# Kernel tuning notes

Hardware: AMD Instinct MI355X
Metric: run time of the kernel (lower is better)

Reference implementation:

```python
import jax, jax.numpy as jnp
import numpy as np

B, SEQ_LEN, CHANNELS, PRED_LEN = 64, 1024, 512, 720
KERNEL = 25
PAD = (KERNEL - 1) // 2  # 12
IN_LEN = SEQ_LEN // 2    # 512
INV_SQRT2 = 1.0 / np.sqrt(2.0).astype(np.float32)


def dct2_ortho_matrix(N):
    # Orthonormal DCT-II basis: X_k = s_k * sum_n x_n cos(pi*(n+0.5)*k/N)
    n = np.arange(N, dtype=np.float64)
    k = np.arange(N, dtype=np.float64)
    M = np.cos(np.pi * (n[None, :] + 0.5) * k[:, None] / N)
    scale = np.sqrt(2.0 / N) * np.ones(N)
    scale[0] = np.sqrt(1.0 / N)
    return jnp.asarray((scale[:, None] * M).astype(np.float32))  # [k, n]


def setup_inputs() -> dict:
    key = jax.random.key(0)
    k1, k2, k3, k4, k5 = jax.random.split(key, 5)
    bound = 1.0 / np.sqrt(IN_LEN)
    return {
        "x": jax.random.normal(k1, (B, SEQ_LEN, CHANNELS), dtype=jnp.float32),
        "W_seasonal": jax.random.uniform(k2, (PRED_LEN, IN_LEN), jnp.float32, -bound, bound),
        "b_seasonal": jax.random.uniform(k3, (PRED_LEN,), jnp.float32, -bound, bound),
        "W_trend": jax.random.uniform(k4, (PRED_LEN, IN_LEN), jnp.float32, -bound, bound),
        "b_trend": jax.random.uniform(k5, (PRED_LEN,), jnp.float32, -bound, bound),
    }


def reference(x, W_seasonal, b_seasonal, W_trend, b_trend):
    # --- series decomposition: moving average (edge-padded, window 25) ---
    padded = jnp.pad(x, ((0, 0), (PAD, PAD), (0, 0)), mode="edge")  # [B, L+24, C]
    cs = jnp.cumsum(padded, axis=1)
    cs = jnp.pad(cs, ((0, 0), (1, 0), (0, 0)))  # leading zero, [B, L+25, C]
    trend = (cs[:, KERNEL:, :] - cs[:, :-KERNEL, :]) / KERNEL  # [B, L, C]
    seasonal = x - trend

    # [B, C, L]
    s = jnp.transpose(seasonal, (0, 2, 1))
    t = jnp.transpose(trend, (0, 2, 1))

    # --- grouped conv1d with [1,1]/sqrt(2), stride 2 (Haar low-pass downsample) ---
    def down(v):
        return (v[..., 0::2] + v[..., 1::2]) * INV_SQRT2  # [B, C, L/2]

    s = down(s)
    t = down(t)

    # --- orthonormal DCT-II over last axis, then divide by length ---
    Mdct = dct2_ortho_matrix(IN_LEN)  # [k, n]
    s = jnp.einsum("bcn,kn->bck", s, Mdct) / IN_LEN
    t = jnp.einsum("bcn,kn->bck", t, Mdct) / IN_LEN

    # --- shared Linear per branch ---
    s_out = jnp.einsum("bck,pk->bcp", s, W_seasonal) + b_seasonal
    t_out = jnp.einsum("bck,pk->bcp", t, W_trend) + b_trend

    out = s_out + t_out  # [B, C, pred_len]
    return jnp.transpose(out, (0, 2, 1))  # [B, pred_len, C]
```

## Files before the change

kernel.cpp:

```cpp
#include <hip/hip_runtime.h>
#include <hip/hip_bf16.h>
#include <math.h>


#define BATCH 64
#define SEQ 1024
#define CH 512
#define PRED 720
#define INV_SQRT2 0.70710678118654752440f

typedef __attribute__((ext_vector_type(4))) float floatx4;
typedef __attribute__((ext_vector_type(8))) short bf16x8;

#define KBF_OFF   0ull
#define BIAS_OFF  1572864ull
#define MW_OFF    1575936ull
#define WEFFS_OFF 2624512ull
#define WEFFT_OFF 4099072ull
#define XT_OFF    5573632ull
#define WS_NEED   (XT_OFF + 67108864ull)

__global__ void build_M(float* __restrict__ Mw) {
    int idx = blockIdx.x * 256 + threadIdx.x;
    int k = idx >> 9, n = idx & 511;
    int m = ((2 * n + 1) * k) & 2047;
    float ang = (float)m * (float)(M_PI / 1024.0);
    float scale = (k == 0) ? 0.04419417382415922f
                           : 0.0625f;
    Mw[idx] = cosf(ang) * scale * (1.0f / 512.0f);
}

__global__ void __launch_bounds__(256) build_weff(
    const float* __restrict__ Ws_in, const float* __restrict__ Wt_in,
    const float* __restrict__ Mw,
    float* __restrict__ outS, float* __restrict__ outT) {
    const float* W = blockIdx.z ? Wt_in : Ws_in;
    float* out     = blockIdx.z ? outT  : outS;
    int n0 = blockIdx.x * 64;
    int p0 = blockIdx.y * 64;
    int t  = threadIdx.x;
    int tx = t & 15, ty = t >> 4;
    __shared__ float wlds[32][65];
    __shared__ float mlds[32][64];
    float a[4][4] = {};
    for (int kb = 0; kb < 512; kb += 32) {
        __syncthreads();
        {
            int pp = t >> 2, kk0 = (t & 3) * 8;
            int prow = min(p0 + pp, PRED - 1);
            const float* wsrc = &W[(size_t)prow * 512 + kb + kk0];
#pragma unroll
            for (int e = 0; e < 8; e++) wlds[kk0 + e][pp] = wsrc[e];
        }
        {
            int kk = t >> 3, nn = (t & 7) * 8;
            const float* msrc = &Mw[(size_t)(kb + kk) * 512 + n0 + nn];
            *reinterpret_cast<floatx4*>(&mlds[kk][nn])     = *reinterpret_cast<const floatx4*>(&msrc[0]);
            *reinterpret_cast<floatx4*>(&mlds[kk][nn + 4]) = *reinterpret_cast<const floatx4*>(&msrc[4]);
        }
        __syncthreads();
#pragma unroll
        for (int kk = 0; kk < 32; kk++) {
            floatx4 wv = *reinterpret_cast<const floatx4*>(&wlds[kk][ty * 4]);
            floatx4 mv = *reinterpret_cast<const floatx4*>(&mlds[kk][tx * 4]);
#pragma unroll
            for (int i = 0; i < 4; i++)
#pragma unroll
                for (int j = 0; j < 4; j++)
                    a[i][j] += wv[i] * mv[j];
        }
    }
#pragma unroll
    for (int i = 0; i < 4; i++) {
        int p = p0 + ty * 4 + i;
        if (p < PRED) {
            floatx4 v = {a[i][0], a[i][1], a[i][2], a[i][3]};
            *reinterpret_cast<floatx4*>(&out[(size_t)p * 512 + n0 + tx * 4]) = v;
        }
    }
}

__device__ __forceinline__ int tcnt(int j, int l) {
    if (l == 0)    return max(0, 13 - j);
    if (l == 1023) return max(0, j - 1010);
    int d = l - j; if (d < 0) d = -d;
    return (d <= 12) ? 1 : 0;
}

__global__ void build_kmat(const float* __restrict__ Ws, const float* __restrict__ Wt,
                           const float* __restrict__ bs, const float* __restrict__ bt,
                           __hip_bfloat16* __restrict__ Kbf, float* __restrict__ bias) {
    int idx = blockIdx.x * 256 + threadIdx.x;
    int p = idx >> 10, l = idx & 1023;
    if (p >= PRED) { Kbf[idx] = __float2bfloat16(0.0f); return; }
    if (l == 0) bias[p] = bs[p] + bt[p];
    float v = INV_SQRT2 * Ws[(size_t)p * 512 + (l >> 1)];
    int jlo = max(0, l - 12), jhi = min(1023, l + 12);
    float acc = 0.f;
    for (int n = (jlo >> 1); n <= (jhi >> 1); n++) {
        int c = tcnt(2 * n, l) + tcnt(2 * n + 1, l);
        if (c) acc += (Wt[(size_t)p * 512 + n] - Ws[(size_t)p * 512 + n]) * (float)c;
    }
    v += acc * (INV_SQRT2 / 25.0f);
    Kbf[idx] = __float2bfloat16(v);
}

__device__ __forceinline__ void async_ld16(const void* g, void* l) {
    __builtin_amdgcn_global_load_lds((const __attribute__((address_space(1))) void*)g,
                                     (__attribute__((address_space(3))) void*)l, 16, 0, 0);
}

__device__ __forceinline__ short f2bf(float f) {
    __hip_bfloat16 h = __float2bfloat16(f);
    return *reinterpret_cast<short*>(&h);
}

__global__ void __launch_bounds__(256) xpose(const float* __restrict__ x,
                                             short* __restrict__ xT) {
    __shared__ float lds[64][65];
    int t = threadIdx.x;
    int l0 = blockIdx.x * 64, c0 = blockIdx.y * 64, b = blockIdx.z;
    const float* xb = x + (size_t)b * SEQ * CH;
    int row4 = t >> 4, cq = t & 15;
#pragma unroll
    for (int i = 0; i < 4; i++) {
        int row = row4 + i * 16;
        floatx4 v = *reinterpret_cast<const floatx4*>(
            xb + (size_t)(l0 + row) * CH + c0 + cq * 4);
#pragma unroll
        for (int e = 0; e < 4; e++) lds[row][cq * 4 + e] = v[e];
    }
    __syncthreads();
    size_t outb = (size_t)b * CH * SEQ;
#pragma unroll
    for (int r = 0; r < 2; r++) {
        int u = r * 256 + t;
        int lr = u & 7, c = u >> 3;
        bf16x8 s;
#pragma unroll
        for (int e = 0; e < 8; e++) s[e] = f2bf(lds[lr * 8 + e][c]);
        *reinterpret_cast<bf16x8*>(&xT[outb + (size_t)(c0 + c) * SEQ + l0 + lr * 8]) = s;
    }
}

__global__ void __launch_bounds__(256, 4) gemm_main_t(
    const short* __restrict__ Kbf, const short* __restrict__ xT,
    const float* __restrict__ bias, float* __restrict__ out) {
    __shared__ __align__(16) short ldsbuf[2 * 2 * 128 * 32];
    int t = threadIdx.x;
    int wave = t >> 6, lane = t & 63;
    int bid = blockIdx.x;
    int work = (bid & 7) * 192 + (bid >> 3);
    int mt = work % 6;
    int grp = work / 6;
    int nt = grp & 3, b = grp >> 2;
    int wm = wave >> 1, wn = wave & 1;
    const short* Ag = Kbf + (size_t)mt * 128 * 1024;
    const short* Bg = xT + ((size_t)b * CH + nt * 128) * 1024;

    size_t srcoff[2];
#pragma unroll
    for (int rdi = 0; rdi < 2; rdi++) {
        int q = rdi * 256 + t;
        int row = ((q >> 6) << 4) + (q & 15);
        int ko = ((q >> 4) & 3) * 8;
        srcoff[rdi] = (size_t)row * 1024 + ko;
    }

    floatx4 acc[4][4];
#pragma unroll
    for (int i = 0; i < 4; i++)
#pragma unroll
        for (int j = 0; j < 4; j++)
            acc[i][j] = (floatx4){0.f, 0.f, 0.f, 0.f};

#pragma unroll
    for (int rdi = 0; rdi < 2; rdi++) {
        char* dA = (char*)ldsbuf + rdi * 4096 + wave * 1024;
        async_ld16(Ag + srcoff[rdi], dA);
        async_ld16(Bg + srcoff[rdi], dA + 8192);
    }
    __syncthreads();

    int cur = 0;
    for (int it = 0; it < 32; ++it) {
        if (it < 31) {
            int k0n = (it + 1) * 32;
            char* base = (char*)ldsbuf + (cur ^ 1) * 16384;
#pragma unroll
            for (int rdi = 0; rdi < 2; rdi++) {
                char* dA = base + rdi * 4096 + wave * 1024;
                async_ld16(Ag + srcoff[rdi] + k0n, dA);
                async_ld16(Bg + srcoff[rdi] + k0n, dA + 8192);
            }
        }
        const char* cb = (const char*)ldsbuf + cur * 16384;
        bf16x8 af[4], bf[4];
#pragma unroll
        for (int i = 0; i < 4; i++)
            af[i] = *reinterpret_cast<const bf16x8*>(cb + ((wm * 4 + i) << 10) + (lane << 4));
#pragma unroll
        for (int j = 0; j < 4; j++)
            bf[j] = *reinterpret_cast<const bf16x8*>(cb + 8192 + ((wn * 4 + j) << 10) + (lane << 4));
#pragma unroll
        for (int i = 0; i < 4; i++)
#pragma unroll
            for (int j = 0; j < 4; j++)
                acc[i][j] = __builtin_amdgcn_mfma_f32_16x16x32_bf16(af[i], bf[j], acc[i][j], 0, 0, 0);
        __syncthreads();
        cur ^= 1;
    }

    int lm = lane & 15, kq = lane >> 4;
    int p0r = mt * 128 + wm * 64;
    int cb2 = nt * 128 + wn * 64 + lm;
    size_t outb = (size_t)b * PRED * CH;
#pragma unroll
    for (int i = 0; i < 4; i++) {
#pragma unroll
        for (int r = 0; r < 4; r++) {
            int p = p0r + i * 16 + kq * 4 + r;
            if (p < PRED) {
                float bv = bias[p];
#pragma unroll
                for (int j = 0; j < 4; j++)
                    __builtin_nontemporal_store(acc[i][j][r] + bv,
                                                &out[outb + (size_t)p * CH + cb2 + j * 16]);
            }
        }
    }
}

__global__ void __launch_bounds__(256) gemm_main(
    const short* __restrict__ Kbf, const float* __restrict__ x,
    const float* __restrict__ bias, float* __restrict__ out) {
    __shared__ __align__(16) short ldsA[128 * 32];
    int t = threadIdx.x;
    int wave = t >> 6, lane = t & 63;
    int mt = blockIdx.x % 6, nt = blockIdx.x / 6;
    int b  = blockIdx.y;
    int wm = wave >> 1, wn = wave & 1;
    const short* Ag = Kbf + (size_t)mt * 128 * 1024;
    const float* xb = x + (size_t)b * SEQ * CH;
    int lm = lane & 15, kq = lane >> 4;
    int cj[4];
    for (int j = 0; j < 4; j++) cj[j] = nt * 128 + wn * 64 + j * 16 + lm;

    floatx4 acc[4][4];
    for (int i = 0; i < 4; i++)
        for (int j = 0; j < 4; j++)
            acc[i][j] = (floatx4){0.f, 0.f, 0.f, 0.f};

    for (int k0 = 0; k0 < 1024; k0 += 32) {
        for (int rdi = 0; rdi < 2; rdi++) {
            int q = rdi * 256 + t;
            int row = q >> 2, ko = (q & 3) * 8;
            async_ld16(Ag + (size_t)row * 1024 + k0 + ko,
                       (char*)ldsA + rdi * 4096 + wave * 1024);
        }
        bf16x8 bfrag[4];
        int krow = k0 + kq * 8;
#pragma unroll
        for (int j = 0; j < 4; j++) {
            const float* xc = xb + (size_t)krow * CH + cj[j];
            bf16x8 bv;
#pragma unroll
            for (int i = 0; i < 8; i++) bv[i] = f2bf(xc[(size_t)i * CH]);
            bfrag[j] = bv;
        }
        __syncthreads();
        bf16x8 af[4];
        for (int i = 0; i < 4; i++)
            af[i] = *(const bf16x8*)&ldsA[(wm * 64 + i * 16 + lm) * 32 + kq * 8];
        for (int i = 0; i < 4; i++)
            for (int j = 0; j < 4; j++)
                acc[i][j] = __builtin_amdgcn_mfma_f32_16x16x32_bf16(af[i], bfrag[j], acc[i][j], 0, 0, 0);
        __syncthreads();
    }

    int p0 = mt * 128 + wm * 64;
    size_t outb = (size_t)b * PRED * CH;
    for (int i = 0; i < 4; i++) {
        for (int r = 0; r < 4; r++) {
            int p = p0 + i * 16 + kq * 4 + r;
            if (p < PRED) {
                float bv = bias[p];
                for (int j = 0; j < 4; j++) {
                    out[outb + (size_t)p * CH + cj[j]] = acc[i][j][r] + bv;
                }
            }
        }
    }
}

extern "C" void kernel_launch(void* const* d_in, const int* in_sizes, int n_in,
                              void* d_out, int out_size, void* d_ws, size_t ws_size,
                              hipStream_t stream) {
    const float* xp = nullptr; const float* wp[2] = {nullptr, nullptr};
    const float* bp[2] = {nullptr, nullptr};
    int wn = 0, bn = 0;
    for (int i = 0; i < n_in; i++) {
        if (in_sizes[i] == 33554432) xp = (const float*)d_in[i];
        else if (in_sizes[i] == 368640 && wn < 2) wp[wn++] = (const float*)d_in[i];
        else if (in_sizes[i] == 720 && bn < 2) bp[bn++] = (const float*)d_in[i];
    }
    if (!xp || wn != 2 || bn != 2) {
        xp = (const float*)d_in[0]; wp[0] = (const float*)d_in[1];
        bp[0] = (const float*)d_in[2]; wp[1] = (const float*)d_in[3];
        bp[1] = (const float*)d_in[4];
    }
    float* out = (float*)d_out;

    char* ws = (char*)d_ws;
    __hip_bfloat16* Kbf = (__hip_bfloat16*)(ws + KBF_OFF);
    float* bias  = (float*)(ws + BIAS_OFF);
    float* Mw    = (float*)(ws + MW_OFF);
    float* WeffS = (float*)(ws + WEFFS_OFF);
    float* WeffT = (float*)(ws + WEFFT_OFF);
    short* xT    = (short*)(ws + XT_OFF);

    bool big = (ws_size >= (size_t)WS_NEED);

    if (big) xpose<<<dim3(16, 8, 64), 256, 0, stream>>>(xp, xT);
    build_M<<<1024, 256, 0, stream>>>(Mw);
    build_weff<<<dim3(8, 12, 2), 256, 0, stream>>>(wp[0], wp[1], Mw, WeffS, WeffT);
    build_kmat<<<3072, 256, 0, stream>>>(WeffS, WeffT, bp[0], bp[1], Kbf, bias);
    if (big)
        gemm_main_t<<<1536, 256, 0, stream>>>((const short*)Kbf, (const short*)xT, bias, out);
    else
        gemm_main<<<dim3(24, 64), 256, 0, stream>>>((const short*)Kbf, xp, bias, out);
}
```

Measured before the change: 379.3 us.

## Triple-buffer GEMM LDS pipeline with single barrier per iteration and MFMA priority

Restructures the main GEMM's K loop from double to triple buffering in LDS, prefetching two stages ahead. Each iteration uses a vmcnt wait plus one barrier instead of a trailing __syncthreads, so global loads have more time to land. MFMA sections get raised wave priority, and the final stage is peeled out of the loop. It also makes the transpose kernel's x loads nontemporal. LDS use grows to 48KB per block and launch bounds drop to 3 blocks per CU, which lowers occupancy.

```diff
diff --git a/kernel.cpp b/kernel.cpp
--- a/kernel.cpp
+++ b/kernel.cpp
@@ -125,8 +125,8 @@
 #pragma unroll
     for (int i = 0; i < 4; i++) {
         int row = row4 + i * 16;
-        floatx4 v = *reinterpret_cast<const floatx4*>(
-            xb + (size_t)(l0 + row) * CH + c0 + cq * 4);
+        floatx4 v = __builtin_nontemporal_load(reinterpret_cast<const floatx4*>(
+            xb + (size_t)(l0 + row) * CH + c0 + cq * 4));
 #pragma unroll
         for (int e = 0; e < 4; e++) lds[row][cq * 4 + e] = v[e];
     }
@@ -143,10 +143,10 @@
     }
 }
 
-__global__ void __launch_bounds__(256, 4) gemm_main_t(
+__global__ void __launch_bounds__(256, 3) gemm_main_t(
     const short* __restrict__ Kbf, const short* __restrict__ xT,
     const float* __restrict__ bias, float* __restrict__ out) {
-    __shared__ __align__(16) short ldsbuf[2 * 2 * 128 * 32];
+    __shared__ __align__(16) short ldsbuf[3 * 2 * 128 * 32];
     int t = threadIdx.x;
     int wave = t >> 6, lane = t & 63;
     int bid = blockIdx.x;
@@ -175,18 +175,25 @@
             acc[i][j] = (floatx4){0.f, 0.f, 0.f, 0.f};
 
 #pragma unroll
-    for (int rdi = 0; rdi < 2; rdi++) {
-        char* dA = (char*)ldsbuf + rdi * 4096 + wave * 1024;
-        async_ld16(Ag + srcoff[rdi], dA);
-        async_ld16(Bg + srcoff[rdi], dA + 8192);
-    }
-    __syncthreads();
-
-    int cur = 0;
-    for (int it = 0; it < 32; ++it) {
-        if (it < 31) {
-            int k0n = (it + 1) * 32;
-            char* base = (char*)ldsbuf + (cur ^ 1) * 16384;
+    for (int s = 0; s < 2; s++) {
+        char* base = (char*)ldsbuf + s * 16384;
+        int k0 = s * 32;
+#pragma unroll
+        for (int rdi = 0; rdi < 2; rdi++) {
+            char* dA = base + rdi * 4096 + wave * 1024;
+            async_ld16(Ag + srcoff[rdi] + k0, dA);
+            async_ld16(Bg + srcoff[rdi] + k0, dA + 8192);
+        }
+    }
+
+    int cur = 0, nx2 = 2;
+    for (int it = 0; it < 31; ++it) {
+        asm volatile("s_waitcnt vmcnt(4)" ::: "memory");
+        __builtin_amdgcn_s_barrier();
+        __builtin_amdgcn_sched_barrier(0);
+        if (it < 30) {
+            int k0n = (it + 2) * 32;
+            char* base = (char*)ldsbuf + nx2 * 16384;
 #pragma unroll
             for (int rdi = 0; rdi < 2; rdi++) {
                 char* dA = base + rdi * 4096 + wave * 1024;
@@ -202,13 +209,33 @@
 #pragma unroll
         for (int j = 0; j < 4; j++)
             bf[j] = *reinterpret_cast<const bf16x8*>(cb + 8192 + ((wn * 4 + j) << 10) + (lane << 4));
+        __builtin_amdgcn_s_setprio(1);
 #pragma unroll
         for (int i = 0; i < 4; i++)
 #pragma unroll
             for (int j = 0; j < 4; j++)
                 acc[i][j] = __builtin_amdgcn_mfma_f32_16x16x32_bf16(af[i], bf[j], acc[i][j], 0, 0, 0);
-        __syncthreads();
-        cur ^= 1;
+        __builtin_amdgcn_s_setprio(0);
+        cur = (cur == 2) ? 0 : cur + 1;
+        nx2 = (nx2 == 2) ? 0 : nx2 + 1;
+    }
+    asm volatile("s_waitcnt vmcnt(0)" ::: "memory");
+    __builtin_amdgcn_s_barrier();
+    __builtin_amdgcn_sched_barrier(0);
+    {
+        const char* cb = (const char*)ldsbuf + cur * 16384;
+        bf16x8 af[4], bf[4];
+#pragma unroll
+        for (int i = 0; i < 4; i++)
+            af[i] = *reinterpret_cast<const bf16x8*>(cb + ((wm * 4 + i) << 10) + (lane << 4));
+#pragma unroll
+        for (int j = 0; j < 4; j++)
+            bf[j] = *reinterpret_cast<const bf16x8*>(cb + 8192 + ((wn * 4 + j) << 10) + (lane << 4));
+#pragma unroll
+        for (int i = 0; i < 4; i++)
+#pragma unroll
+            for (int j = 0; j < 4; j++)
+                acc[i][j] = __builtin_amdgcn_mfma_f32_16x16x32_bf16(af[i], bf[j], acc[i][j], 0, 0, 0);
     }
 
     int lm = lane & 15, kq = lane >> 4;
```

After: 368.0 us. 3.0% less time.
